# Kernel optimization log

Measured on AMD Instinct MI355X. Metric: run time of the kernel, lower is better.

Reference implementation:

```python
import jax, jax.numpy as jnp
import numpy as np
import math

D_MODEL = 1024
N_HEADS = 16
N_QUBITS = 8
HEAD_DIM = D_MODEL // N_HEADS
B, L = 2, 2048


def setup_inputs() -> dict:
    key = jax.random.key(0)
    ks = jax.random.split(key, 16)
    s = 0.02
    return {
        "query": jax.random.normal(ks[0], (B, L, D_MODEL), jnp.float32),
        "key_": jax.random.normal(ks[1], (B, L, D_MODEL), jnp.float32),
        "value": jax.random.normal(ks[2], (B, L, D_MODEL), jnp.float32),
        "Wq": jax.random.normal(ks[3], (D_MODEL, D_MODEL), jnp.float32) * s,
        "bq": jnp.zeros((D_MODEL,), jnp.float32),
        "Wk": jax.random.normal(ks[4], (D_MODEL, D_MODEL), jnp.float32) * s,
        "bk": jnp.zeros((D_MODEL,), jnp.float32),
        "Wv": jax.random.normal(ks[5], (D_MODEL, D_MODEL), jnp.float32) * s,
        "bv": jnp.zeros((D_MODEL,), jnp.float32),
        "Wo": jax.random.normal(ks[6], (D_MODEL, D_MODEL), jnp.float32) * s,
        "bo": jnp.zeros((D_MODEL,), jnp.float32),
        "Wf": jax.random.normal(ks[7], (HEAD_DIM, N_QUBITS), jnp.float32) * s,  # feature map weight (input->qubits)
        "bf": jnp.zeros((N_QUBITS,), jnp.float32),
        "quantum_weights": jax.random.normal(ks[8], (N_HEADS, N_QUBITS), jnp.float32) * 0.1,
        "entanglement_strength": jnp.asarray(0.5, jnp.float32),
    }


def _heads(x):
    # [B, L, D] -> [B, H, L, head_dim]
    b, l, _ = x.shape
    return x.reshape(b, l, N_HEADS, HEAD_DIM).transpose(0, 2, 1, 3)


def reference(query, key_, value, Wq, bq, Wk, bk, Wv, bv, Wo, bo, Wf, bf, quantum_weights, entanglement_strength):
    Qh = _heads(query @ Wq.T + bq)   # [B,H,L,d]
    Kh = _heads(key_ @ Wk.T + bk)
    Vh = _heads(value @ Wv.T + bv)

    classical = jnp.einsum("bhid,bhjd->bhij", Qh, Kh) / math.sqrt(HEAD_DIM)

    # quantum feature map: tanh(linear) -> [B,H,L,Q]
    qq = jnp.tanh(jnp.einsum("bhld,dq->bhlq", Qh, Wf) + bf)
    kq = jnp.tanh(jnp.einsum("bhld,dq->bhlq", Kh, Wf) + bf)

    # mean_q w_q*cos(qq_i - kq_j) == (1/Q)[(w*cos qq)@cos(kq)^T + (w*sin qq)@sin(kq)^T]
    w = jax.nn.sigmoid(quantum_weights)[None, :, None, :]  # [1,H,1,Q]
    quantum = (
        jnp.einsum("bhiq,bhjq->bhij", jnp.cos(qq) * w, jnp.cos(kq))
        + jnp.einsum("bhiq,bhjq->bhij", jnp.sin(qq) * w, jnp.sin(kq))
    ) / N_QUBITS
    ent = jax.nn.sigmoid(entanglement_strength)
    quantum = quantum * ent

    mix = ent  # same sigmoid(entanglement_strength) used as mixing weight
    combined = (1.0 - mix) * classical + mix * quantum

    attn = jax.nn.softmax(combined, axis=-1)  # [B,H,L,L]
    attended = jnp.einsum("bhij,bhjd->bhid", attn, Vh)
    attended = attended.transpose(0, 2, 1, 3).reshape(query.shape[0], query.shape[1], D_MODEL)
    output = attended @ Wo.T + bo
    return output, attn.mean(axis=1)
```

## Files before the change

kernel.cpp:

```cpp
#include <hip/hip_runtime.h>


typedef unsigned short u16;
typedef unsigned int u32;
typedef short v8s __attribute__((ext_vector_type(8)));
typedef float v4f __attribute__((ext_vector_type(4)));

static __device__ __forceinline__ float b2f(u16 h) {
  union { u32 u; float f; } a; a.u = ((u32)h) << 16; return a.f;
}
static __device__ __forceinline__ u16 f2b(float f) {
  union { float f; u32 u; } a; a.f = f;
  u32 u = a.u;
  u32 r = u + 0x7FFFu + ((u >> 16) & 1u);
  return (u16)(r >> 16);
}
static __device__ __forceinline__ v4f mfma16(v8s a, v8s b, v4f c) {
  return __builtin_amdgcn_mfma_f32_16x16x32_bf16(a, b, c, 0, 0, 0);
}
static __device__ __forceinline__ void gload16(const u16* g, u16* l) {
  __builtin_amdgcn_global_load_lds((const __attribute__((address_space(1))) u32*)g,
                                   (__attribute__((address_space(3))) u32*)l, 16, 0, 0);
}
static __device__ __forceinline__ float exp2fast(float x) {
  float r; asm("v_exp_f32 %0, %1" : "=v"(r) : "v"(x)); return r;
}
static __device__ __forceinline__ u32 cvtpk_bf16(float lo, float hi) {
  u32 r; asm("v_cvt_pk_bf16_f32 %0, %1, %2" : "=v"(r) : "v"(lo), "v"(hi)); return r;
}

__global__ __launch_bounds__(256) void k_f2b_all(const float* __restrict__ q, const float* __restrict__ k,
                                                 const float* __restrict__ v, const float* __restrict__ wq,
                                                 const float* __restrict__ wk, const float* __restrict__ wv,
                                                 const float* __restrict__ wo, u16* __restrict__ y) {
  int i = blockIdx.x * 256 + threadIdx.x;
  const float* src; int off;
  if (i < 1048576)      { src = q;  off = i; }
  else if (i < 2097152) { src = k;  off = i - 1048576; }
  else if (i < 3145728) { src = v;  off = i - 2097152; }
  else if (i < 3407872) { src = wq; off = i - 3145728; }
  else if (i < 3670016) { src = wk; off = i - 3407872; }
  else if (i < 3932160) { src = wv; off = i - 3670016; }
  else                  { src = wo; off = i - 3932160; }
  float4 val = ((const float4*)src)[off];
  union { u16 s[4]; uint2 u; } o;
  o.s[0] = f2b(val.x); o.s[1] = f2b(val.y); o.s[2] = f2b(val.z); o.s[3] = f2b(val.w);
  ((uint2*)y)[i] = o.u;
}

__global__ __launch_bounds__(256) void k_gemm128(
    const u16* __restrict__ A0, const u16* __restrict__ A1, const u16* __restrict__ A2,
    const u16* __restrict__ B0, const u16* __restrict__ B1, const u16* __restrict__ B2,
    const float* __restrict__ bias0, const float* __restrict__ bias1, const float* __restrict__ bias2,
    u16* __restrict__ O0, u16* __restrict__ O1, u16* __restrict__ O2t,
    float* __restrict__ Cf) {
  __shared__ __align__(16) u16 pool[18432];
  u16* As = pool;
  u16* Bs = pool + 8192;
  const int K = 1024, N = 1024;
  int t = threadIdx.x, w = t >> 6, lane = t & 63, quad = lane >> 4, l16 = lane & 15;
  int z = blockIdx.z;
  const u16* A = (z == 0) ? A0 : (z == 1) ? A1 : A2;
  const u16* Bm = (z == 0) ? B0 : (z == 1) ? B1 : B2;
  const float* bias = (z == 0) ? bias0 : (z == 1) ? bias1 : bias2;
  int n0 = blockIdx.x * 128, m0 = blockIdx.y * 128;

  int srow = lane >> 2, scol = (lane & 3) * 8;
  const u16* gp[8]; u16* lp[8];
#pragma unroll
  for (int qi = 0; qi < 8; ++qi) {
    int mat = qi >> 2, kk = (qi >> 1) & 1, g = w + (qi & 1) * 4;
    int row = g * 16 + srow;
    gp[qi] = (mat ? Bm + (size_t)(n0 + row) * K : A + (size_t)(m0 + row) * K) + kk * 32 + scol;
    lp[qi] = (mat ? Bs : As) + kk * 4096 + g * 512;
  }

  int mrow = (w >> 1) * 64, ncol = (w & 1) * 64;
  v4f zf = {0.f, 0.f, 0.f, 0.f};
  v4f acc[4][4];
#pragma unroll
  for (int mi = 0; mi < 4; ++mi)
#pragma unroll
    for (int ni = 0; ni < 4; ++ni) acc[mi][ni] = zf;

  for (int k0 = 0; k0 < K; k0 += 64) {
    __syncthreads();
#pragma unroll
    for (int qi = 0; qi < 8; ++qi) gload16(gp[qi] + k0, lp[qi]);
    __syncthreads();
#pragma unroll
    for (int kk = 0; kk < 2; ++kk) {
      v8s af[4], bfr[4];
#pragma unroll
      for (int x = 0; x < 4; ++x) {
        af[x] = *(const v8s*)&As[kk * 4096 + (mrow + x * 16 + l16) * 32 + quad * 8];
        bfr[x] = *(const v8s*)&Bs[kk * 4096 + (ncol + x * 16 + l16) * 32 + quad * 8];
      }
#pragma unroll
      for (int mi = 0; mi < 4; ++mi)
#pragma unroll
        for (int ni = 0; ni < 4; ++ni)
          acc[mi][ni] = mfma16(af[mi], bfr[ni], acc[mi][ni]);
    }
  }

  float bv[4];
#pragma unroll
  for (int ni = 0; ni < 4; ++ni) bv[ni] = bias[n0 + ncol + ni * 16 + l16];

  if (Cf) {
#pragma unroll
    for (int mi = 0; mi < 4; ++mi)
#pragma unroll
      for (int ni = 0; ni < 4; ++ni)
#pragma unroll
        for (int r = 0; r < 4; ++r)
          Cf[(size_t)(m0 + mrow + mi * 16 + quad * 4 + r) * N + n0 + ncol + ni * 16 + l16] =
              acc[mi][ni][r] + bv[ni];
  } else if (z != 2) {
    u16* O = z ? O1 : O0;
#pragma unroll
    for (int mi = 0; mi < 4; ++mi)
#pragma unroll
      for (int ni = 0; ni < 4; ++ni)
#pragma unroll
        for (int r = 0; r < 4; ++r)
          O[(size_t)(m0 + mrow + mi * 16 + quad * 4 + r) * N + n0 + ncol + ni * 16 + l16] =
              f2b(acc[mi][ni][r] + bv[ni]);
  } else {
    __syncthreads();
    u16* Ts = pool + w * 64 * 68;
#pragma unroll
    for (int mi = 0; mi < 4; ++mi)
#pragma unroll
      for (int ni = 0; ni < 4; ++ni)
#pragma unroll
        for (int r = 0; r < 4; ++r)
          Ts[(mi * 16 + quad * 4 + r) * 68 + ni * 16 + l16] = f2b(acc[mi][ni][r] + bv[ni]);
    int c = lane;
    union { uint4 u[8]; u16 s[64]; } cb;
#pragma unroll
    for (int e = 0; e < 64; ++e) cb.s[e] = Ts[e * 68 + c];
    int bb = m0 >> 11, ml = m0 & 2047;
    u16* dst = O2t + ((size_t)(bb * 1024 + n0 + ncol + c)) * 2048 + ml + mrow;
#pragma unroll
    for (int e = 0; e < 8; ++e) *(uint4*)(dst + e * 8) = cb.u[e];
  }
}

__global__ __launch_bounds__(256) void k_features(const u16* __restrict__ Qp, const u16* __restrict__ Kp,
                                                  const float* __restrict__ Wf, const float* __restrict__ bff,
                                                  const float* __restrict__ qw, const float* __restrict__ entp,
                                                  u16* __restrict__ Qaa, u16* __restrict__ Kaa) {
  int isK = blockIdx.y;
  const u16* P = isK ? Kp : Qp;
  u16* Out = isK ? Kaa : Qaa;
  int idx = blockIdx.x * 256 + threadIdx.x;
  int b = idx >> 15, h = (idx >> 11) & 15, l = idx & 2047;
  const u16* src = P + ((size_t)(b * 2048 + l)) * 1024 + h * 64;
  u16* dst = Out + (size_t)idx * 96;
  const float4* Wf4 = (const float4*)Wf;

  float x[64];
#pragma unroll
  for (int g = 0; g < 8; ++g) {
    union { uint4 u; u16 s[8]; } uu;
    uu.u = *(const uint4*)(src + g * 8);
#pragma unroll
    for (int e = 0; e < 8; ++e) x[g * 8 + e] = b2f(uu.s[e]);
  }
  float qv[8];
#pragma unroll
  for (int qq = 0; qq < 8; ++qq) qv[qq] = bff[qq];
#pragma unroll
  for (int d = 0; d < 64; ++d) {
    float4 wa = Wf4[d * 2], wb = Wf4[d * 2 + 1];
    float xd = x[d];
    qv[0] += xd * wa.x; qv[1] += xd * wa.y; qv[2] += xd * wa.z; qv[3] += xd * wa.w;
    qv[4] += xd * wb.x; qv[5] += xd * wb.y; qv[6] += xd * wb.z; qv[7] += xd * wb.w;
  }
  float cs[8], sn[8];
#pragma unroll
  for (int qq = 0; qq < 8; ++qq) {
    float e2 = __expf(2.f * qv[qq]);
    float th = 1.f - 2.f / (e2 + 1.f);
    __sincosf(th, &sn[qq], &cs[qq]);
  }
  float ent = 1.f / (1.f + __expf(-entp[0]));
  union { uint4 u; u16 s[8]; } pc, ps;
  if (!isK) {
#pragma unroll
    for (int g = 0; g < 8; ++g) *(uint4*)(dst + g * 8) = *(const uint4*)(src + g * 8);
#pragma unroll
    for (int qq = 0; qq < 8; ++qq) {
      float sw = 1.f / (1.f + __expf(-qw[h * 8 + qq]));
      pc.s[qq] = f2b(cs[qq] * sw);
      ps.s[qq] = f2b(sn[qq] * sw);
    }
  } else {
    const float LOG2E = 1.44269504088896f;
    float c1 = (1.f - ent) * 0.125f * LOG2E, c2 = ent * ent * 0.125f * LOG2E;
#pragma unroll
    for (int g = 0; g < 8; ++g) {
      union { uint4 u; u16 s[8]; } ob;
#pragma unroll
      for (int e = 0; e < 8; ++e) ob.s[e] = f2b(x[g * 8 + e] * c1);
      *(uint4*)(dst + g * 8) = ob.u;
    }
#pragma unroll
    for (int qq = 0; qq < 8; ++qq) {
      pc.s[qq] = f2b(cs[qq] * c2);
      ps.s[qq] = f2b(sn[qq] * c2);
    }
  }
  *(uint4*)(dst + 64) = pc.u;
  *(uint4*)(dst + 72) = ps.u;
  uint4 z4 = {0, 0, 0, 0};
  *(uint4*)(dst + 80) = z4;
  *(uint4*)(dst + 88) = z4;
}

__global__ __launch_bounds__(256, 4) void k_flash(const u16* __restrict__ Qa, const u16* __restrict__ Ka,
                                                  const u16* __restrict__ VtG, u16* __restrict__ At,
                                                  float* __restrict__ lb) {
  __shared__ __align__(16) u16 Ks[2][6144];
  __shared__ __align__(16) u16 Ps[4][16][72];

  int t = threadIdx.x, w = t >> 6, lane = t & 63, quad = lane >> 4, l16 = lane & 15;
  int i0 = blockIdx.x * 64, h = blockIdx.y, b = blockIdx.z;
  size_t qbase = ((size_t)(b * 16 + h)) * 2048 * 96;
  const u16* Kbase = Ka + qbase;
  const u16* Vbase = VtG + ((size_t)(b * 1024 + h * 64)) * 2048;

  int goff = w * 512 + lane * 8;
  int loff = w * 512;

#pragma unroll
  for (int p = 0; p < 3; ++p)
    gload16(Kbase + p * 2048 + goff, &Ks[0][p * 2048 + loff]);

  v8s aq[3];
  {
    const u16* Qrow = Qa + qbase + (size_t)(i0 + w * 16 + l16) * 96;
#pragma unroll
    for (int ks = 0; ks < 3; ++ks) aq[ks] = *(const v8s*)(Qrow + ks * 32 + quad * 8);
  }

  v4f zf = {0.f, 0.f, 0.f, 0.f};
  v4f oacc[4] = {zf, zf, zf, zf};
  float l_acc = 0.f;

  __syncthreads();

  for (int j0 = 0; j0 < 2048; j0 += 64) {
    int cur = (j0 >> 6) & 1;
    const u16* kb = Ks[cur];

    v8s vf[8];
#pragma unroll
    for (int idx = 0; idx < 8; ++idx)
      vf[idx] = *(const v8s*)(Vbase + (size_t)((idx >> 1) * 16 + l16) * 2048 + j0 +
                              (idx & 1) * 32 + quad * 8);
    if (j0 + 64 < 2048) {
      const u16* src = Kbase + (size_t)(j0 + 64) * 96;
#pragma unroll
      for (int p = 0; p < 3; ++p)
        gload16(src + p * 2048 + goff, &Ks[cur ^ 1][p * 2048 + loff]);
    }

    v4f sacc[4] = {zf, zf, zf, zf};
    __builtin_amdgcn_s_setprio(1);
#pragma unroll
    for (int j16 = 0; j16 < 4; ++j16)
#pragma unroll
      for (int ks = 0; ks < 3; ++ks) {
        v8s kf = *(const v8s*)(kb + (j16 * 16 + l16) * 96 + ks * 32 + quad * 8);
        sacc[j16] = mfma16(kf, aq[ks], sacc[j16]);
      }
    __builtin_amdgcn_s_setprio(0);

#pragma unroll
    for (int j16 = 0; j16 < 4; ++j16) {
      float e0 = exp2fast(sacc[j16][0]);
      float e1 = exp2fast(sacc[j16][1]);
      float e2 = exp2fast(sacc[j16][2]);
      float e3 = exp2fast(sacc[j16][3]);
      l_acc += (e0 + e1) + (e2 + e3);
      uint2 pp;
      pp.x = cvtpk_bf16(e0, e1);
      pp.y = cvtpk_bf16(e2, e3);
      *(uint2*)&Ps[w][l16][j16 * 16 + quad * 4] = pp;
    }

    __builtin_amdgcn_s_setprio(1);
#pragma unroll
    for (int jh = 0; jh < 2; ++jh) {
      v8s pf = *(const v8s*)&Ps[w][l16][jh * 32 + quad * 8];
#pragma unroll
      for (int d16 = 0; d16 < 4; ++d16)
        oacc[d16] = mfma16(pf, vf[d16 * 2 + jh], oacc[d16]);
    }
    __builtin_amdgcn_s_setprio(0);
    __syncthreads();
  }

  l_acc += __shfl_xor(l_acc, 16, 64);
  l_acc += __shfl_xor(l_acc, 32, 64);
  float linv = 1.f / l_acc;
#pragma unroll
  for (int r = 0; r < 4; ++r) {
    float li = __shfl(linv, quad * 4 + r, 64);
    int ri = i0 + w * 16 + quad * 4 + r;
#pragma unroll
    for (int d16 = 0; d16 < 4; ++d16)
      At[((size_t)(b * 2048 + ri)) * 1024 + h * 64 + d16 * 16 + l16] = f2b(oacc[d16][r] * li);
  }
  if (lane < 16) {
    size_t mbase = ((size_t)(b * 16 + h)) * 2048;
    lb[mbase + i0 + w * 16 + lane] = l_acc;
  }
}

__global__ __launch_bounds__(256) void k_pass2(const u16* __restrict__ Qa, const u16* __restrict__ Ka,
                                               const float* __restrict__ lb,
                                               float* __restrict__ out1) {
  __shared__ __align__(16) u16 Ks[64][104];
  __shared__ float Ls[16][128];
  int t = threadIdx.x, w = t >> 6, lane = t & 63, quad = lane >> 4, l16 = lane & 15;
  int j0 = blockIdx.x * 64, i0 = blockIdx.y * 128, b = blockIdx.z;

#pragma unroll
  for (int rep = 0; rep < 8; ++rep) {
    int idx = t + rep * 256;
    int hh = idx >> 7, il = idx & 127;
    Ls[hh][il] = 0.0625f / lb[((size_t)(b * 16 + hh)) * 2048 + i0 + il];
  }

  size_t base0 = (size_t)b * 16 * 2048 * 96;
  const u16* kg[3]; u16* kd[3];
#pragma unroll
  for (int rep = 0; rep < 3; ++rep) {
    int idx = t + rep * 256;
    int r_ = idx / 12, c_ = idx % 12;
    kg[rep] = Ka + base0 + (size_t)(j0 + r_) * 96 + c_ * 8;
    kd[rep] = &Ks[r_][c_ * 8];
  }
  uint4 f0 = *(const uint4*)kg[0];
  uint4 f1 = *(const uint4*)kg[1];
  uint4 f2 = *(const uint4*)kg[2];

  const u16* q0 = Qa + base0 + (size_t)(i0 + w * 32 + l16) * 96 + quad * 8;
  const u16* q1 = q0 + 16 * 96;

  v4f zf = {0.f, 0.f, 0.f, 0.f};
  v4f macc[2][4];
#pragma unroll
  for (int i16 = 0; i16 < 2; ++i16)
#pragma unroll
    for (int j16 = 0; j16 < 4; ++j16) macc[i16][j16] = zf;

  v8s a[2][3];
#pragma unroll
  for (int ks = 0; ks < 3; ++ks) {
    a[0][ks] = *(const v8s*)(q0 + ks * 32);
    a[1][ks] = *(const v8s*)(q1 + ks * 32);
  }

  for (int h = 0; h < 16; ++h) {
    *(uint4*)kd[0] = f0;
    *(uint4*)kd[1] = f1;
    *(uint4*)kd[2] = f2;
    __syncthreads();
    if (h < 15) {
      kg[0] += 196608; kg[1] += 196608; kg[2] += 196608;
      f0 = *(const uint4*)kg[0];
      f1 = *(const uint4*)kg[1];
      f2 = *(const uint4*)kg[2];
    }

    v4f sacc[2][4];
#pragma unroll
    for (int i16 = 0; i16 < 2; ++i16)
#pragma unroll
      for (int j16 = 0; j16 < 4; ++j16) sacc[i16][j16] = zf;
#pragma unroll
    for (int ks = 0; ks < 3; ++ks)
#pragma unroll
      for (int j16 = 0; j16 < 4; ++j16) {
        v8s kf = *(const v8s*)&Ks[j16 * 16 + l16][ks * 32 + quad * 8];
        sacc[0][j16] = mfma16(a[0][ks], kf, sacc[0][j16]);
        sacc[1][j16] = mfma16(a[1][ks], kf, sacc[1][j16]);
      }

    if (h < 15) {
      q0 += 196608; q1 += 196608;
#pragma unroll
      for (int ks = 0; ks < 3; ++ks) {
        a[0][ks] = *(const v8s*)(q0 + ks * 32);
        a[1][ks] = *(const v8s*)(q1 + ks * 32);
      }
    }

    float li[2][4];
#pragma unroll
    for (int i16 = 0; i16 < 2; ++i16)
#pragma unroll
      for (int r = 0; r < 4; ++r)
        li[i16][r] = Ls[h][w * 32 + i16 * 16 + quad * 4 + r];
#pragma unroll
    for (int i16 = 0; i16 < 2; ++i16)
#pragma unroll
      for (int j16 = 0; j16 < 4; ++j16)
#pragma unroll
        for (int r = 0; r < 4; ++r)
          macc[i16][j16][r] += exp2fast(sacc[i16][j16][r]) * li[i16][r];
    __syncthreads();
  }

  float* o = out1 + (size_t)b * 2048 * 2048;
#pragma unroll
  for (int i16 = 0; i16 < 2; ++i16)
#pragma unroll
    for (int j16 = 0; j16 < 4; ++j16)
#pragma unroll
      for (int r = 0; r < 4; ++r)
        o[(size_t)(i0 + w * 32 + i16 * 16 + quad * 4 + r) * 2048 + j0 + j16 * 16 + l16] =
            macc[i16][j16][r];
}

extern "C" void kernel_launch(void* const* d_in, const int* in_sizes, int n_in,
                              void* d_out, int out_size, void* d_ws, size_t ws_size,
                              hipStream_t stream) {
  (void)in_sizes; (void)n_in; (void)out_size; (void)ws_size;
  const float* query = (const float*)d_in[0];
  const float* key_  = (const float*)d_in[1];
  const float* value = (const float*)d_in[2];
  const float* Wq = (const float*)d_in[3];
  const float* bq = (const float*)d_in[4];
  const float* Wk = (const float*)d_in[5];
  const float* bk = (const float*)d_in[6];
  const float* Wv = (const float*)d_in[7];
  const float* bv = (const float*)d_in[8];
  const float* Wo = (const float*)d_in[9];
  const float* bo = (const float*)d_in[10];
  const float* Wf = (const float*)d_in[11];
  const float* bff = (const float*)d_in[12];
  const float* qw = (const float*)d_in[13];
  const float* entp = (const float*)d_in[14];

  char* p = (char*)d_ws;
  u16* Xq  = (u16*)(p + 0);
  u16* Xk  = (u16*)(p + 8388608);
  u16* Xv  = (u16*)(p + 16777216);
  u16* Wqb = (u16*)(p + 25165824);
  u16* Wkb = (u16*)(p + 27262976);
  u16* Wvb = (u16*)(p + 29360128);
  u16* Qp  = (u16*)(p + 33554432);
  u16* Kp  = (u16*)(p + 41943040);
  u16* VtG = (u16*)(p + 50331648);
  u16* Qaa = (u16*)(p + 58720256);
  u16* Kaa = (u16*)(p + 71303168);
  float* lb = (float*)(p + 84148224);
  u16* At  = (u16*)(p + 84410368);
  u16* Wob = (u16*)(p + 31457280);

  k_f2b_all<<<16384, 256, 0, stream>>>(query, key_, value, Wq, Wk, Wv, Wo, Xq);

  k_gemm128<<<dim3(8, 32, 3), 256, 0, stream>>>(Xq, Xk, Xv, Wqb, Wkb, Wvb, bq, bk, bv,
                                                Qp, Kp, VtG, nullptr);

  k_features<<<dim3(256, 2), 256, 0, stream>>>(Qp, Kp, Wf, bff, qw, entp, Qaa, Kaa);

  k_flash<<<dim3(32, 16, 2), 256, 0, stream>>>(Qaa, Kaa, VtG, At, lb);

  k_pass2<<<dim3(32, 16, 2), 256, 0, stream>>>(Qaa, Kaa, lb, (float*)d_out + 4194304);

  k_gemm128<<<dim3(8, 32, 1), 256, 0, stream>>>(At, At, At, Wob, Wob, Wob, bo, bo, bo,
                                                nullptr, nullptr, nullptr, (float*)d_out);
}
```

Measured before the change: 392.7 us.

## Register-stage K/V prefetch with padded LDS rows in flash kernel

Replaces the direct global-to-LDS loads of K with a register-staged two-deep prefetch: K tiles are loaded into registers two iterations ahead and written into a padded LDS layout (row stride 104) to reduce bank conflicts. V fragments for the next tile are also prefetched into registers one iteration ahead. The occupancy hint in launch_bounds is dropped. This aims to hide global load latency behind the MFMA work, at the cost of higher register pressure and possibly lower occupancy.

```diff
diff --git a/kernel.cpp b/kernel.cpp
--- a/kernel.cpp
+++ b/kernel.cpp
@@ -220,52 +220,77 @@
   *(uint4*)(dst + 88) = z4;
 }
 
-__global__ __launch_bounds__(256, 4) void k_flash(const u16* __restrict__ Qa, const u16* __restrict__ Ka,
-                                                  const u16* __restrict__ VtG, u16* __restrict__ At,
-                                                  float* __restrict__ lb) {
-  __shared__ __align__(16) u16 Ks[2][6144];
+__global__ __launch_bounds__(256) void k_flash(const u16* __restrict__ Qa, const u16* __restrict__ Ka,
+                                               const u16* __restrict__ VtG, u16* __restrict__ At,
+                                               float* __restrict__ lb) {
+  __shared__ __align__(16) u16 Ks[2][64][104];
   __shared__ __align__(16) u16 Ps[4][16][72];
 
   int t = threadIdx.x, w = t >> 6, lane = t & 63, quad = lane >> 4, l16 = lane & 15;
   int i0 = blockIdx.x * 64, h = blockIdx.y, b = blockIdx.z;
   size_t qbase = ((size_t)(b * 16 + h)) * 2048 * 96;
-  const u16* Kbase = Ka + qbase;
-  const u16* Vbase = VtG + ((size_t)(b * 1024 + h * 64)) * 2048;
-
-  int goff = w * 512 + lane * 8;
-  int loff = w * 512;
-
-#pragma unroll
-  for (int p = 0; p < 3; ++p)
-    gload16(Kbase + p * 2048 + goff, &Ks[0][p * 2048 + loff]);
-
   v8s aq[3];
   {
     const u16* Qrow = Qa + qbase + (size_t)(i0 + w * 16 + l16) * 96;
 #pragma unroll
     for (int ks = 0; ks < 3; ++ks) aq[ks] = *(const v8s*)(Qrow + ks * 32 + quad * 8);
   }
+  const u16* Kbase = Ka + qbase;
+  const u16* Vbase = VtG + ((size_t)(b * 1024 + h * 64)) * 2048;
+
+  const u16* kg[3]; int kdo[3];
+#pragma unroll
+  for (int p = 0; p < 3; ++p) {
+    int idx = t + p * 256, r_ = idx / 12, c_ = idx % 12;
+    kg[p] = Kbase + (size_t)r_ * 96 + c_ * 8;
+    kdo[p] = r_ * 104 + c_ * 8;
+  }
+  u16* ks0 = &Ks[0][0][0];
+  u16* ks1 = &Ks[1][0][0];
 
   v4f zf = {0.f, 0.f, 0.f, 0.f};
   v4f oacc[4] = {zf, zf, zf, zf};
   float l_acc = 0.f;
 
+  uint4 fk0 = *(const uint4*)kg[0];
+  uint4 fk1 = *(const uint4*)kg[1];
+  uint4 fk2 = *(const uint4*)kg[2];
+  kg[0] += 6144; kg[1] += 6144; kg[2] += 6144;
+  *(uint4*)(ks0 + kdo[0]) = fk0;
+  *(uint4*)(ks0 + kdo[1]) = fk1;
+  *(uint4*)(ks0 + kdo[2]) = fk2;
+  fk0 = *(const uint4*)kg[0];
+  fk1 = *(const uint4*)kg[1];
+  fk2 = *(const uint4*)kg[2];
+  kg[0] += 6144; kg[1] += 6144; kg[2] += 6144;
+  v8s vf[8];
+#pragma unroll
+  for (int idx = 0; idx < 8; ++idx)
+    vf[idx] = *(const v8s*)(Vbase + (size_t)((idx >> 1) * 16 + l16) * 2048 + (idx & 1) * 32 + quad * 8);
   __syncthreads();
 
   for (int j0 = 0; j0 < 2048; j0 += 64) {
     int cur = (j0 >> 6) & 1;
-    const u16* kb = Ks[cur];
-
-    v8s vf[8];
-#pragma unroll
-    for (int idx = 0; idx < 8; ++idx)
-      vf[idx] = *(const v8s*)(Vbase + (size_t)((idx >> 1) * 16 + l16) * 2048 + j0 +
-                              (idx & 1) * 32 + quad * 8);
-    if (j0 + 64 < 2048) {
-      const u16* src = Kbase + (size_t)(j0 + 64) * 96;
-#pragma unroll
-      for (int p = 0; p < 3; ++p)
-        gload16(src + p * 2048 + goff, &Ks[cur ^ 1][p * 2048 + loff]);
+    const u16* kb = cur ? ks1 : ks0;
+    u16* kw = cur ? ks0 : ks1;
+    bool more = (j0 + 64) < 2048;
+    if (more) {
+      *(uint4*)(kw + kdo[0]) = fk0;
+      *(uint4*)(kw + kdo[1]) = fk1;
+      *(uint4*)(kw + kdo[2]) = fk2;
+    }
+    if (j0 + 128 < 2048) {
+      fk0 = *(const uint4*)kg[0];
+      fk1 = *(const uint4*)kg[1];
+      fk2 = *(const uint4*)kg[2];
+      kg[0] += 6144; kg[1] += 6144; kg[2] += 6144;
+    }
+    v8s vn[8];
+    if (more) {
+#pragma unroll
+      for (int idx = 0; idx < 8; ++idx)
+        vn[idx] = *(const v8s*)(Vbase + (size_t)((idx >> 1) * 16 + l16) * 2048 + j0 + 64 +
+                                (idx & 1) * 32 + quad * 8);
     }
 
     v4f sacc[4] = {zf, zf, zf, zf};
@@ -274,7 +299,7 @@
     for (int j16 = 0; j16 < 4; ++j16)
 #pragma unroll
       for (int ks = 0; ks < 3; ++ks) {
-        v8s kf = *(const v8s*)(kb + (j16 * 16 + l16) * 96 + ks * 32 + quad * 8);
+        v8s kf = *(const v8s*)(kb + (j16 * 16 + l16) * 104 + ks * 32 + quad * 8);
         sacc[j16] = mfma16(kf, aq[ks], sacc[j16]);
       }
     __builtin_amdgcn_s_setprio(0);
@@ -301,7 +326,11 @@
         oacc[d16] = mfma16(pf, vf[d16 * 2 + jh], oacc[d16]);
     }
     __builtin_amdgcn_s_setprio(0);
-    __syncthreads();
+    if (more) {
+#pragma unroll
+      for (int idx = 0; idx < 8; ++idx) vf[idx] = vn[idx];
+      __syncthreads();
+    }
   }
 
   l_acc += __shfl_xor(l_acc, 16, 64);
```

Measured after the change: 429.9 us. 1.09x slower.

## Split flash KV across waves with LDS-staged swizzled V and XCD-aware block mapping

Applied to the files above, without the earlier changes.

The flash kernel changes from one 16-row query slice per wave to each wave covering all 64 query rows on a 16-key slice of every tile. K and V are staged into swizzled LDS with async global-to-LDS loads, and the P fragments stay in registers across pairs of tiles instead of passing through LDS. Partial outputs and row sums are reduced across waves through LDS at the end. Both flash and pass2 now launch 1D grids remapped so neighbouring head/batch tiles land on the same XCD for L2 reuse, and pass2 double-buffers its K tile so it needs one barrier per head. The costs are more registers (occupancy hint lowered from 4 to 3) and an extra cross-wave reduction epilogue.

```diff
diff --git a/kernel.cpp b/kernel.cpp
--- a/kernel.cpp
+++ b/kernel.cpp
@@ -4,6 +4,7 @@
 typedef unsigned short u16;
 typedef unsigned int u32;
 typedef short v8s __attribute__((ext_vector_type(8)));
+typedef short v4s __attribute__((ext_vector_type(4)));
 typedef float v4f __attribute__((ext_vector_type(4)));
 
 static __device__ __forceinline__ float b2f(u16 h) {
@@ -220,114 +221,197 @@
   *(uint4*)(dst + 88) = z4;
 }
 
-__global__ __launch_bounds__(256, 4) void k_flash(const u16* __restrict__ Qa, const u16* __restrict__ Ka,
+__global__ __launch_bounds__(256, 3) void k_flash(const u16* __restrict__ Qa, const u16* __restrict__ Ka,
                                                   const u16* __restrict__ VtG, u16* __restrict__ At,
                                                   float* __restrict__ lb) {
-  __shared__ __align__(16) u16 Ks[2][6144];
-  __shared__ __align__(16) u16 Ps[4][16][72];
+  __shared__ __align__(16) u16 pool[25088];
+  u16* KsP = pool;
+  u16* VsP = pool + 16384;
+  float* Lred = (float*)(pool + 24576);
 
   int t = threadIdx.x, w = t >> 6, lane = t & 63, quad = lane >> 4, l16 = lane & 15;
-  int i0 = blockIdx.x * 64, h = blockIdx.y, b = blockIdx.z;
+  int bid = blockIdx.x;
+  int sem = ((bid & 7) << 7) | (bid >> 3);
+  int i0 = (sem & 31) << 6;
+  int hb = sem >> 5;
+  int h = hb & 15, b = hb >> 4;
   size_t qbase = ((size_t)(b * 16 + h)) * 2048 * 96;
   const u16* Kbase = Ka + qbase;
   const u16* Vbase = VtG + ((size_t)(b * 1024 + h * 64)) * 2048;
 
-  int goff = w * 512 + lane * 8;
-  int loff = w * 512;
-
-#pragma unroll
-  for (int p = 0; p < 3; ++p)
-    gload16(Kbase + p * 2048 + goff, &Ks[0][p * 2048 + loff]);
-
-  v8s aq[3];
-  {
-    const u16* Qrow = Qa + qbase + (size_t)(i0 + w * 16 + l16) * 96;
-#pragma unroll
-    for (int ks = 0; ks < 3; ++ks) aq[ks] = *(const v8s*)(Qrow + ks * 32 + quad * 8);
-  }
+  v8s aq[4][3];
+#pragma unroll
+  for (int i16 = 0; i16 < 4; ++i16) {
+    const u16* Qrow = Qa + qbase + (size_t)(i0 + i16 * 16 + l16) * 96;
+#pragma unroll
+    for (int ks = 0; ks < 3; ++ks) aq[i16][ks] = *(const v8s*)(Qrow + ks * 32 + quad * 8);
+  }
+
+  int kun = (t & 15) ^ ((t >> 4) & 7);
+  const u16* kg0 = Kbase + (size_t)(t >> 4) * 96 + kun * 8;
+  int vun = (t & 7) ^ ((t >> 3) & 7);
+  const u16* vg0 = Vbase + (size_t)(t >> 3) * 2048 + vun * 8;
+  u16* kld0 = KsP + w * 512;
+  u16* vld0 = VsP + w * 512;
 
   v4f zf = {0.f, 0.f, 0.f, 0.f};
-  v4f oacc[4] = {zf, zf, zf, zf};
-  float l_acc = 0.f;
-
+  v4f oacc[4][4];
+#pragma unroll
+  for (int i16 = 0; i16 < 4; ++i16)
+#pragma unroll
+    for (int d16 = 0; d16 < 4; ++d16) oacc[i16][d16] = zf;
+  float lp[4] = {0.f, 0.f, 0.f, 0.f};
+
+#pragma unroll
+  for (int p = 0; p < 4; ++p) gload16(kg0 + p * 1536, kld0 + p * 2048);
+#pragma unroll
+  for (int p = 0; p < 2; ++p) gload16(vg0 + p * 65536, vld0 + p * 2048);
   __syncthreads();
+
+  int kxor = (l16 & 7) * 8;
+  int krd = (w * 16 + l16) * 128;
+  int vxor = (((2 * w + (quad >> 1)) ^ (l16 & 7)) * 8) + (quad & 1) * 4;
+
+  v4s paE[4], vbE[4];
 
   for (int j0 = 0; j0 < 2048; j0 += 64) {
     int cur = (j0 >> 6) & 1;
-    const u16* kb = Ks[cur];
-
-    v8s vf[8];
-#pragma unroll
-    for (int idx = 0; idx < 8; ++idx)
-      vf[idx] = *(const v8s*)(Vbase + (size_t)((idx >> 1) * 16 + l16) * 2048 + j0 +
-                              (idx & 1) * 32 + quad * 8);
+    const u16* kb = KsP + cur * 8192;
+    const u16* vt = VsP + cur * 4096;
     if (j0 + 64 < 2048) {
-      const u16* src = Kbase + (size_t)(j0 + 64) * 96;
-#pragma unroll
-      for (int p = 0; p < 3; ++p)
-        gload16(src + p * 2048 + goff, &Ks[cur ^ 1][p * 2048 + loff]);
+      int nb = cur ^ 1;
+#pragma unroll
+      for (int p = 0; p < 4; ++p)
+        gload16(kg0 + p * 1536 + (size_t)(j0 + 64) * 96, kld0 + p * 2048 + nb * 8192);
+#pragma unroll
+      for (int p = 0; p < 2; ++p)
+        gload16(vg0 + p * 65536 + (j0 + 64), vld0 + p * 2048 + nb * 4096);
     }
 
     v4f sacc[4] = {zf, zf, zf, zf};
     __builtin_amdgcn_s_setprio(1);
 #pragma unroll
-    for (int j16 = 0; j16 < 4; ++j16)
-#pragma unroll
-      for (int ks = 0; ks < 3; ++ks) {
-        v8s kf = *(const v8s*)(kb + (j16 * 16 + l16) * 96 + ks * 32 + quad * 8);
-        sacc[j16] = mfma16(kf, aq[ks], sacc[j16]);
+    for (int ks = 0; ks < 3; ++ks) {
+      v8s kf = *(const v8s*)(kb + krd + (((ks * 4 + quad) * 8) ^ kxor));
+#pragma unroll
+      for (int i16 = 0; i16 < 4; ++i16) sacc[i16] = mfma16(kf, aq[i16][ks], sacc[i16]);
+    }
+    __builtin_amdgcn_s_setprio(0);
+
+    v4s vbc[4];
+#pragma unroll
+    for (int d16 = 0; d16 < 4; ++d16)
+      vbc[d16] = *(const v4s*)(vt + (d16 * 16 + l16) * 64 + vxor);
+
+    v4s pac[4];
+#pragma unroll
+    for (int i16 = 0; i16 < 4; ++i16) {
+      float e0 = exp2fast(sacc[i16][0]);
+      float e1 = exp2fast(sacc[i16][1]);
+      float e2 = exp2fast(sacc[i16][2]);
+      float e3 = exp2fast(sacc[i16][3]);
+      lp[i16] += (e0 + e1) + (e2 + e3);
+      union { u32 u[2]; v4s s; } pa;
+      pa.u[0] = cvtpk_bf16(e0, e1);
+      pa.u[1] = cvtpk_bf16(e2, e3);
+      pac[i16] = pa.s;
+    }
+
+    if ((j0 & 64) == 0) {
+#pragma unroll
+      for (int x = 0; x < 4; ++x) { paE[x] = pac[x]; vbE[x] = vbc[x]; }
+    } else {
+      v8s bfr[4];
+#pragma unroll
+      for (int d16 = 0; d16 < 4; ++d16)
+        bfr[d16] = __builtin_shufflevector(vbE[d16], vbc[d16], 0, 1, 2, 3, 4, 5, 6, 7);
+      __builtin_amdgcn_s_setprio(1);
+#pragma unroll
+      for (int i16 = 0; i16 < 4; ++i16) {
+        v8s af = __builtin_shufflevector(paE[i16], pac[i16], 0, 1, 2, 3, 4, 5, 6, 7);
+#pragma unroll
+        for (int d16 = 0; d16 < 4; ++d16)
+          oacc[i16][d16] = mfma16(af, bfr[d16], oacc[i16][d16]);
       }
-    __builtin_amdgcn_s_setprio(0);
-
-#pragma unroll
-    for (int j16 = 0; j16 < 4; ++j16) {
-      float e0 = exp2fast(sacc[j16][0]);
-      float e1 = exp2fast(sacc[j16][1]);
-      float e2 = exp2fast(sacc[j16][2]);
-      float e3 = exp2fast(sacc[j16][3]);
-      l_acc += (e0 + e1) + (e2 + e3);
-      uint2 pp;
-      pp.x = cvtpk_bf16(e0, e1);
-      pp.y = cvtpk_bf16(e2, e3);
-      *(uint2*)&Ps[w][l16][j16 * 16 + quad * 4] = pp;
-    }
-
-    __builtin_amdgcn_s_setprio(1);
-#pragma unroll
-    for (int jh = 0; jh < 2; ++jh) {
-      v8s pf = *(const v8s*)&Ps[w][l16][jh * 32 + quad * 8];
+      __builtin_amdgcn_s_setprio(0);
+    }
+    __syncthreads();
+  }
+
+#pragma unroll
+  for (int i16 = 0; i16 < 4; ++i16) {
+    lp[i16] += __shfl_xor(lp[i16], 16, 64);
+    lp[i16] += __shfl_xor(lp[i16], 32, 64);
+  }
+  if (lane < 16) {
+#pragma unroll
+    for (int i16 = 0; i16 < 4; ++i16) Lred[(w * 4 + i16) * 16 + lane] = lp[i16];
+  }
+  __syncthreads();
+  float ls = Lred[(0 * 4 + w) * 16 + l16] + Lred[(1 * 4 + w) * 16 + l16] +
+             Lred[(2 * 4 + w) * 16 + l16] + Lred[(3 * 4 + w) * 16 + l16];
+  if (lane < 16) lb[((size_t)(b * 16 + h)) * 2048 + i0 + w * 16 + lane] = ls;
+  float linv = 1.f / ls;
+  float lr[4];
+#pragma unroll
+  for (int r = 0; r < 4; ++r) lr[r] = __shfl(linv, quad * 4 + r, 64);
+
+  v4f own[4];
+#pragma unroll
+  for (int d16 = 0; d16 < 4; ++d16) {
+    v4f s01 = (w & 1) ? oacc[1][d16] : oacc[0][d16];
+    v4f s23 = (w & 1) ? oacc[3][d16] : oacc[2][d16];
+    own[d16] = (w & 2) ? s23 : s01;
+  }
+
+  float* OredF = (float*)pool;
+#pragma unroll
+  for (int ph = 0; ph < 2; ++ph) {
+    int t0 = ph * 2;
+#pragma unroll
+    for (int tg = 0; tg < 2; ++tg) {
+      int tgt = t0 + tg;
+      if (w != tgt) {
+        int si = w - (w > tgt ? 1 : 0);
+        int base = (tg * 3 + si) * 16;
+#pragma unroll
+        for (int d16 = 0; d16 < 4; ++d16)
+#pragma unroll
+          for (int r = 0; r < 4; ++r)
+            OredF[(base + quad * 4 + r) * 66 + d16 * 16 + l16] = oacc[tgt][d16][r];
+      }
+    }
+    __syncthreads();
+    if (w >= t0 && w < t0 + 2) {
+      int sb = (w - t0) * 3;
 #pragma unroll
       for (int d16 = 0; d16 < 4; ++d16)
-        oacc[d16] = mfma16(pf, vf[d16 * 2 + jh], oacc[d16]);
-    }
-    __builtin_amdgcn_s_setprio(0);
-    __syncthreads();
-  }
-
-  l_acc += __shfl_xor(l_acc, 16, 64);
-  l_acc += __shfl_xor(l_acc, 32, 64);
-  float linv = 1.f / l_acc;
-#pragma unroll
-  for (int r = 0; r < 4; ++r) {
-    float li = __shfl(linv, quad * 4 + r, 64);
-    int ri = i0 + w * 16 + quad * 4 + r;
-#pragma unroll
-    for (int d16 = 0; d16 < 4; ++d16)
-      At[((size_t)(b * 2048 + ri)) * 1024 + h * 64 + d16 * 16 + l16] = f2b(oacc[d16][r] * li);
-  }
-  if (lane < 16) {
-    size_t mbase = ((size_t)(b * 16 + h)) * 2048;
-    lb[mbase + i0 + w * 16 + lane] = l_acc;
+#pragma unroll
+        for (int r = 0; r < 4; ++r) {
+          float s = own[d16][r];
+#pragma unroll
+          for (int si = 0; si < 3; ++si)
+            s += OredF[((sb + si) * 16 + quad * 4 + r) * 66 + d16 * 16 + l16];
+          int ri = i0 + w * 16 + quad * 4 + r;
+          At[((size_t)(b * 2048 + ri)) * 1024 + h * 64 + d16 * 16 + l16] = f2b(s * lr[r]);
+        }
+    }
+    if (ph == 0) __syncthreads();
   }
 }
 
 __global__ __launch_bounds__(256) void k_pass2(const u16* __restrict__ Qa, const u16* __restrict__ Ka,
                                                const float* __restrict__ lb,
                                                float* __restrict__ out1) {
-  __shared__ __align__(16) u16 Ks[64][104];
+  __shared__ __align__(16) u16 Ks[2][64][104];
   __shared__ float Ls[16][128];
   int t = threadIdx.x, w = t >> 6, lane = t & 63, quad = lane >> 4, l16 = lane & 15;
-  int j0 = blockIdx.x * 64, i0 = blockIdx.y * 128, b = blockIdx.z;
+  int bid = blockIdx.x;
+  int sem = ((bid & 7) << 7) | (bid >> 3);
+  int xcd = sem >> 7;
+  int b = xcd >> 2;
+  int i0 = ((((xcd & 3) << 2) | (sem & 3))) << 7;
+  int j0 = ((sem >> 2) & 31) << 6;
 
 #pragma unroll
   for (int rep = 0; rep < 8; ++rep) {
@@ -343,11 +427,16 @@
     int idx = t + rep * 256;
     int r_ = idx / 12, c_ = idx % 12;
     kg[rep] = Ka + base0 + (size_t)(j0 + r_) * 96 + c_ * 8;
-    kd[rep] = &Ks[r_][c_ * 8];
-  }
+    kd[rep] = &Ks[0][r_][c_ * 8];
+  }
+  const int KSTRIDE = 64 * 104;
+
   uint4 f0 = *(const uint4*)kg[0];
   uint4 f1 = *(const uint4*)kg[1];
   uint4 f2 = *(const uint4*)kg[2];
+  *(uint4*)kd[0] = f0; *(uint4*)kd[1] = f1; *(uint4*)kd[2] = f2;
+  kg[0] += 196608; kg[1] += 196608; kg[2] += 196608;
+  f0 = *(const uint4*)kg[0]; f1 = *(const uint4*)kg[1]; f2 = *(const uint4*)kg[2];
 
   const u16* q0 = Qa + base0 + (size_t)(i0 + w * 32 + l16) * 96 + quad * 8;
   const u16* q1 = q0 + 16 * 96;
@@ -365,18 +454,20 @@
     a[0][ks] = *(const v8s*)(q0 + ks * 32);
     a[1][ks] = *(const v8s*)(q1 + ks * 32);
   }
+  __syncthreads();
 
   for (int h = 0; h < 16; ++h) {
-    *(uint4*)kd[0] = f0;
-    *(uint4*)kd[1] = f1;
-    *(uint4*)kd[2] = f2;
-    __syncthreads();
     if (h < 15) {
+      int aoff = ((h & 1) ^ 1) * KSTRIDE;
+      *(uint4*)(kd[0] + aoff) = f0;
+      *(uint4*)(kd[1] + aoff) = f1;
+      *(uint4*)(kd[2] + aoff) = f2;
+    }
+    if (h < 14) {
       kg[0] += 196608; kg[1] += 196608; kg[2] += 196608;
-      f0 = *(const uint4*)kg[0];
-      f1 = *(const uint4*)kg[1];
-      f2 = *(const uint4*)kg[2];
-    }
+      f0 = *(const uint4*)kg[0]; f1 = *(const uint4*)kg[1]; f2 = *(const uint4*)kg[2];
+    }
+    const u16* Kb = &Ks[h & 1][0][0];
 
     v4f sacc[2][4];
 #pragma unroll
@@ -387,7 +478,7 @@
     for (int ks = 0; ks < 3; ++ks)
 #pragma unroll
       for (int j16 = 0; j16 < 4; ++j16) {
-        v8s kf = *(const v8s*)&Ks[j16 * 16 + l16][ks * 32 + quad * 8];
+        v8s kf = *(const v8s*)(Kb + (j16 * 16 + l16) * 104 + ks * 32 + quad * 8);
         sacc[0][j16] = mfma16(a[0][ks], kf, sacc[0][j16]);
         sacc[1][j16] = mfma16(a[1][ks], kf, sacc[1][j16]);
       }
@@ -471,9 +562,9 @@
 
   k_features<<<dim3(256, 2), 256, 0, stream>>>(Qp, Kp, Wf, bff, qw, entp, Qaa, Kaa);
 
-  k_flash<<<dim3(32, 16, 2), 256, 0, stream>>>(Qaa, Kaa, VtG, At, lb);
-
-  k_pass2<<<dim3(32, 16, 2), 256, 0, stream>>>(Qaa, Kaa, lb, (float*)d_out + 4194304);
+  k_flash<<<dim3(1024), 256, 0, stream>>>(Qaa, Kaa, VtG, At, lb);
+
+  k_pass2<<<dim3(1024), 256, 0, stream>>>(Qaa, Kaa, lb, (float*)d_out + 4194304);
 
   k_gemm128<<<dim3(8, 32, 1), 256, 0, stream>>>(At, At, At, Wob, Wob, Wob, bo, bo, bo,
                                                 nullptr, nullptr, nullptr, (float*)d_out);
```

Result: slower. 1.066 ms (+171.6%).
